# Performance work log

Hardware: AMD Instinct MI355X
Metric: run time of the kernel (lower is better)

Reference implementation:

```python
import jax, jax.numpy as jnp
import numpy as np

B, L, LH, D, H = 32, 512, 2048, 1024, 4
DK = D // H  # dot-attn head dim
NEG = -1e9


def _ln(x, g, b, eps=1e-5):
    m = x.mean(-1, keepdims=True)
    v = ((x - m) ** 2).mean(-1, keepdims=True)
    return (x - m) / jnp.sqrt(v + eps) * g + b


def setup_inputs() -> dict:
    key = jax.random.key(0)
    ks = jax.random.split(key, 16)
    s = 0.05
    inp = {
        "seq_emb": jax.random.normal(ks[0], (B, L, D), jnp.float32),
        "seq_mask": jnp.ones((B, L), jnp.float32),
        "his_seq_emb": jax.random.normal(ks[1], (B, LH, D), jnp.float32),
        "his_seq_mask": jnp.ones((B, LH), jnp.float32),
        # dot-product MHA (bias=True)
        "sa_wq": jax.random.normal(ks[2], (D, D), jnp.float32) * s,
        "sa_bq": jnp.zeros((D,), jnp.float32),
        "sa_wk": jax.random.normal(ks[3], (D, D), jnp.float32) * s,
        "sa_bk": jnp.zeros((D,), jnp.float32),
        "sa_wv": jax.random.normal(ks[4], (D, D), jnp.float32) * s,
        "sa_bv": jnp.zeros((D,), jnp.float32),
        "sa_wo": jax.random.normal(ks[5], (D, D), jnp.float32) * s,
        "sa_bo": jnp.zeros((D,), jnp.float32),
        # short LayerNorm
        "sn_g": jnp.ones((D,), jnp.float32),
        "sn_b": jnp.zeros((D,), jnp.float32),
        # additive MHA (h=1, bias=False)
        "aa_wq": jax.random.normal(ks[6], (D, D), jnp.float32) * s,
        "aa_wk": jax.random.normal(ks[7], (D, D), jnp.float32) * s,
        "aa_wv": jax.random.normal(ks[8], (D, D), jnp.float32) * s,
        "aa_wo": jax.random.normal(ks[9], (D, D), jnp.float32) * s,
        "aa_wa": jax.random.normal(ks[10], (D,), jnp.float32) * s,
        # long LayerNorm
        "ln_g": jnp.ones((D,), jnp.float32),
        "ln_b": jnp.zeros((D,), jnp.float32),
    }
    return inp


def reference(seq_emb, seq_mask, his_seq_emb, his_seq_mask,
              sa_wq, sa_bq, sa_wk, sa_bk, sa_wv, sa_bv, sa_wo, sa_bo,
              sn_g, sn_b, aa_wq, aa_wk, aa_wv, aa_wo, aa_wa, ln_g, ln_b):
    # ---- dot-product self attention over seq_emb (dropout = eval/no-op) ----
    def split_heads(x):  # (B,L,D) -> (B,H,L,DK)
        return x.reshape(B, -1, H, DK).transpose(0, 2, 1, 3)

    q = split_heads(seq_emb @ sa_wq + sa_bq)
    k = split_heads(seq_emb @ sa_wk + sa_bk)
    v = split_heads(seq_emb @ sa_wv + sa_bv)
    scores = jnp.einsum('bhqd,bhkd->bhqk', q, k) / jnp.sqrt(jnp.float32(DK))
    scores = jnp.where(seq_mask[:, None, None, :] == 0, NEG, scores)
    p_attn = jax.nn.softmax(scores, axis=-1)  # (B,H,L,L)
    ctx = jnp.einsum('bhqk,bhkd->bhqd', p_attn, v)
    ctx = ctx.transpose(0, 2, 1, 3).reshape(B, L, D)
    sa_out = ctx @ sa_wo + sa_bo

    poi_attn = _ln(sa_out, sn_g, sn_b) * seq_mask[:, :, None]
    poi_hidden = poi_attn.mean(axis=1, keepdims=True)  # (B,1,D)

    # ---- additive (Bahdanau) attention, h=1, Lq=1 ----
    aq = poi_hidden @ aa_wq        # (B,1,D)
    ak = his_seq_emb @ aa_wk       # (B,LH,D)
    av = his_seq_emb @ aa_wv       # (B,LH,D)
    feats = jnp.tanh(aq[:, :, None, :] + ak[:, None, :, :])  # (B,1,LH,D)
    a_scores = jnp.einsum('bqkd,d->bqk', feats, aa_wa)        # (B,1,LH)
    a_scores = jnp.where(his_seq_mask[:, None, :] == 0, NEG, a_scores)
    a_w = jax.nn.softmax(a_scores, axis=-1)
    a_ctx = jnp.einsum('bqk,bkd->bqd', a_w, av)               # (B,1,D)
    aa_out = a_ctx @ aa_wo

    his_poi_hidden = poi_hidden + _ln(aa_out, ln_g, ln_b)     # (B,1,D)

    attn_weight = p_attn[:, 0, :, :]                          # (B,L,L)
    seq_hidden = jnp.concatenate([poi_hidden, his_poi_hidden], axis=-1)[:, 0, :]  # (B,2D)
    return seq_hidden, attn_weight
```

## Files before the change

kernel.cpp:

```cpp
#include <hip/hip_runtime.h>

#define NEGV (-1000000000.0f)

typedef __attribute__((ext_vector_type(8))) short sh8;
typedef __attribute__((ext_vector_type(4))) short sh4;
typedef __attribute__((ext_vector_type(8))) __bf16 bf16x8;
typedef __attribute__((ext_vector_type(4))) float f32x4;

__device__ __forceinline__ float b2f(unsigned short u) {
  unsigned v = ((unsigned)u) << 16;
  return __builtin_bit_cast(float, v);
}
__device__ __forceinline__ unsigned short f2b(float f) {
  unsigned x = __builtin_bit_cast(unsigned, f);
  unsigned r = (x + 0x7fffu + ((x >> 16) & 1u)) >> 16;
  return (unsigned short)r;
}
__device__ __forceinline__ void g2l16(const void* g, void* l) {
  __builtin_amdgcn_global_load_lds((const __attribute__((address_space(1))) unsigned int*)g,
                                   (__attribute__((address_space(3))) unsigned int*)l, 16, 0, 0);
}
__device__ __forceinline__ f32x4 mfma16(bf16x8 a, bf16x8 b, f32x4 c) {
  return __builtin_amdgcn_mfma_f32_16x16x32_bf16(a, b, c, 0, 0, 0);
}
__device__ __forceinline__ float fast_tanh(float x) {
  x = fminf(fmaxf(x, -15.f), 15.f);
  float e = __expf(2.f * x);
  return (e - 1.f) / (e + 1.f);
}

__global__ void cvt_bf16(const float* __restrict__ src, unsigned short* __restrict__ dst, int n4) {
  int i = blockIdx.x * blockDim.x + threadIdx.x;
  int stride = gridDim.x * blockDim.x;
  for (; i < n4; i += stride) {
    float4 v = ((const float4*)src)[i];
    sh4 o;
    o[0] = (short)f2b(v.x); o[1] = (short)f2b(v.y);
    o[2] = (short)f2b(v.z); o[3] = (short)f2b(v.w);
    ((sh4*)dst)[i] = o;
  }
}

__global__ void tcvt(const float* __restrict__ src, unsigned short* __restrict__ dst) {
  __shared__ float tile[64][65];
  int bx = blockIdx.x, by = blockIdx.y;
  int tx = threadIdx.x & 63, ty = threadIdx.x >> 6;
#pragma unroll
  for (int i = 0; i < 16; ++i) {
    int r = i * 4 + ty;
    tile[r][tx] = src[(size_t)(by * 64 + r) * 1024 + bx * 64 + tx];
  }
  __syncthreads();
#pragma unroll
  for (int i = 0; i < 16; ++i) {
    int r = i * 4 + ty;
    dst[(size_t)(bx * 64 + r) * 1024 + by * 64 + tx] = f2b(tile[tx][r]);
  }
}

template<int EPI>
__global__ __launch_bounds__(512, 1)
void gemm256(const unsigned short* __restrict__ A, const unsigned short* __restrict__ Bt,
             int nbx,
             const float* __restrict__ b0, const float* __restrict__ b1,
             const float* __restrict__ b2,
             unsigned short* __restrict__ O0, unsigned short* __restrict__ O1,
             unsigned short* __restrict__ O2,
             const float* __restrict__ aq, const float* __restrict__ wa,
             float* __restrict__ sc)
{
  __shared__ char lds[131072];
  const int tid = threadIdx.x;
  const int w = tid >> 6, l = tid & 63;
  const int wm = w >> 2, wn = w & 3;
  const int lr = l & 15, g = l >> 4;
  const int swz = (lr >> 1) & 3;

  const int wg = blockIdx.x;
  const int cpx = gridDim.x >> 3;
  const int wgid = (wg & 7) * cpx + (wg >> 3);
  const int bx = wgid % nbx, by = wgid / nbx;
  const size_t m0 = (size_t)by * 256;
  const int n0 = bx * 256;

  f32x4 acc[8][4] = {};
  bf16x8 fa[2][8], fb[2][4];

  const int srow = tid >> 2;
  const int sk = (((tid & 3) ^ ((tid >> 3) & 3)) * 8);
  const unsigned short* gA = A + (m0 + srow) * 1024 + sk;
  const unsigned short* gB = Bt + ((size_t)n0 + srow) * 1024 + sk;
  char* const sbase = lds + w * 1024;

  const int aoff = (wm * 128 + lr) * 64 + ((g ^ swz) * 16);
  const int boff = 16384 + (wn * 64 + lr) * 64 + ((g ^ swz) * 16);

  auto stageAB = [&](int kt) {
    const unsigned short* a = gA + kt * 32;
    const unsigned short* b = gB + kt * 32;
    char* base = sbase + ((kt & 3) << 15);
    g2l16(a, base);
    g2l16(a + 128 * 1024, base + 8192);
    g2l16(b, base + 16384);
    g2l16(b + 128 * 1024, base + 24576);
  };

  stageAB(0); stageAB(1); stageAB(2);
  asm volatile("s_waitcnt vmcnt(4)" ::: "memory");
  __builtin_amdgcn_s_barrier();
  {
    const char* p0 = lds;
#pragma unroll
    for (int j = 0; j < 4; ++j) fb[0][j] = *(const bf16x8*)(p0 + boff + j * 1024);
#pragma unroll
    for (int i = 0; i < 8; ++i) fa[0][i] = *(const bf16x8*)(p0 + aoff + i * 1024);
  }
  __builtin_amdgcn_sched_barrier(0);

#define GITER(KTV, CUR, NXT)                                                   \
  {                                                                            \
    const int kt_ = (KTV);                                                     \
    if (kt_ < 29) stageAB(kt_ + 3);                                            \
    if (kt_ < 31) {                                                            \
      const char* pn_ = lds + (((kt_ + 1) & 3) << 15);                         \
      _Pragma("unroll")                                                        \
      for (int j = 0; j < 4; ++j)                                              \
        fb[NXT][j] = *(const bf16x8*)(pn_ + boff + j * 1024);                  \
      _Pragma("unroll")                                                        \
      for (int i = 0; i < 8; ++i)                                              \
        fa[NXT][i] = *(const bf16x8*)(pn_ + aoff + i * 1024);                  \
    }                                                                          \
    __builtin_amdgcn_sched_barrier(0);                                         \
    __builtin_amdgcn_s_setprio(1);                                             \
    _Pragma("unroll")                                                          \
    for (int i = 0; i < 8; ++i)                                                \
      _Pragma("unroll")                                                        \
      for (int j = 0; j < 4; ++j)                                              \
        acc[i][j] = mfma16(fa[CUR][i], fb[CUR][j], acc[i][j]);                 \
    __builtin_amdgcn_s_setprio(0);                                             \
    if (kt_ < 29) { asm volatile("s_waitcnt vmcnt(4)" ::: "memory"); }         \
    else if (kt_ == 29) { asm volatile("s_waitcnt vmcnt(0)" ::: "memory"); }   \
    if (kt_ < 31) __builtin_amdgcn_s_barrier();                                \
  }

#pragma unroll 1
  for (int kk = 0; kk < 28; kk += 2) {
    GITER(kk, 0, 1)
    GITER(kk + 1, 1, 0)
  }
  GITER(28, 0, 1)
  GITER(29, 1, 0)
  GITER(30, 0, 1)
  GITER(31, 1, 0)
#undef GITER

  if (EPI == 0) {
#pragma unroll
    for (int j = 0; j < 4; ++j) {
      int col = n0 + wn * 64 + j * 16 + lr;
      float bv = b0[col];
#pragma unroll
      for (int i = 0; i < 8; ++i) {
        size_t rowb = m0 + wm * 128 + i * 16 + g * 4;
#pragma unroll
        for (int r = 0; r < 4; ++r)
          O0[(rowb + r) * 1024 + col] = f2b(acc[i][j][r] + bv);
      }
    }
  } else if (EPI == 1) {
#pragma unroll
    for (int j = 0; j < 4; ++j) {
      int col3 = n0 + wn * 64 + j * 16 + lr;
      int part = col3 >> 10, c = col3 & 1023;
      float bv = (part == 0) ? b0[c] : (part == 1) ? b1[c] : b2[c];
      if (part < 2) {
        unsigned short* O = part == 0 ? O0 : O1;
#pragma unroll
        for (int i = 0; i < 8; ++i) {
          size_t rowb = m0 + wm * 128 + i * 16 + g * 4;
#pragma unroll
          for (int r = 0; r < 4; ++r)
            O[(rowb + r) * 1024 + c] = f2b(acc[i][j][r] + bv);
        }
      } else {
        int h = c >> 8, d = c & 255;
#pragma unroll
        for (int i = 0; i < 8; ++i) {
          size_t row = m0 + wm * 128 + i * 16 + g * 4;
          int bb = (int)(row >> 9), ll = (int)(row & 511);
          size_t base = ((size_t)(bb * 4 + h) * 256 + d) * 512 + ll;
#pragma unroll
          for (int r = 0; r < 4; ++r)
            O2[base + r] = f2b(acc[i][j][r] + bv);
        }
      }
    }
  } else {
    const int bb = (int)(m0 >> 11);
#pragma unroll
    for (int i = 0; i < 8; ++i) {
      float rp[4] = {0.f, 0.f, 0.f, 0.f};
#pragma unroll
      for (int j = 0; j < 4; ++j) {
        int col = n0 + wn * 64 + j * 16 + lr;
        float wav = wa[col];
        float aqv = aq[bb * 1024 + col];
#pragma unroll
        for (int r = 0; r < 4; ++r)
          rp[r] += wav * fast_tanh(acc[i][j][r] + aqv);
      }
#pragma unroll
      for (int off = 1; off < 16; off <<= 1)
#pragma unroll
        for (int r = 0; r < 4; ++r)
          rp[r] += __shfl_xor(rp[r], off, 64);
      if (lr == 0) {
        size_t rowb = m0 + wm * 128 + i * 16 + g * 4;
#pragma unroll
        for (int r = 0; r < 4; ++r)
          atomicAdd(&sc[rowb + r], rp[r]);
      }
    }
  }
}

__global__ __launch_bounds__(256, 4)
void attn_kernel(const unsigned short* __restrict__ q, const unsigned short* __restrict__ k,
                 const unsigned short* __restrict__ vT, const float* __restrict__ seq_mask,
                 unsigned short* __restrict__ ctx, float* __restrict__ attn_out)
{
  __shared__ char smem[34304];
  unsigned short* Qs = (unsigned short*)smem;
  unsigned short* Ps = (unsigned short*)smem;
  float* redm = (float*)(smem + 33280);
  float* reds = (float*)(smem + 33792);
  const int t = threadIdx.x, w = t >> 6, l = t & 63;
  const int lr = l & 15, g = l >> 4, lk8 = g * 8;
  const int wg = blockIdx.x;
  const int wgid = (wg & 7) * 256 + (wg >> 3);
  const int qt = wgid & 15, bh = wgid >> 4;
  const int h = bh & 3, b = bh >> 2;
  const int l0 = qt * 32;

  for (int idx = t; idx < 32 * 32; idx += 256) {
    int r = idx >> 5, ch = (idx & 31) * 8;
    *(sh8*)&Qs[r * 264 + ch] =
        *(const sh8*)&q[((size_t)(b * 512 + l0 + r)) * 1024 + h * 256 + ch];
  }
  __syncthreads();

  f32x4 accs[2][8] = {};
  const unsigned short* kbase = k + ((size_t)b * 512) * 1024 + h * 256;
#pragma unroll
  for (int ds = 0; ds < 8; ++ds) {
    int d0 = ds * 32;
    bf16x8 a0 = *(const bf16x8*)&Qs[lr * 264 + d0 + lk8];
    bf16x8 a1 = *(const bf16x8*)&Qs[(16 + lr) * 264 + d0 + lk8];
#pragma unroll
    for (int j = 0; j < 8; ++j) {
      int kj = w * 128 + j * 16 + lr;
      bf16x8 bb = *(const bf16x8*)&kbase[(size_t)kj * 1024 + d0 + lk8];
      accs[0][j] = mfma16(a0, bb, accs[0][j]);
      accs[1][j] = mfma16(a1, bb, accs[1][j]);
    }
  }

#pragma unroll
  for (int j = 0; j < 8; ++j) {
    int col = w * 128 + j * 16 + lr;
    float mv = seq_mask[b * 512 + col];
    bool msk = (mv == 0.f);
#pragma unroll
    for (int i = 0; i < 2; ++i)
#pragma unroll
      for (int r = 0; r < 4; ++r)
        accs[i][j][r] = msk ? NEGV : accs[i][j][r] * 0.0625f;
  }

  float mx[2][4], sm[2][4];
#pragma unroll
  for (int i = 0; i < 2; ++i)
#pragma unroll
    for (int r = 0; r < 4; ++r) {
      float m = accs[i][0][r];
#pragma unroll
      for (int j = 1; j < 8; ++j) m = fmaxf(m, accs[i][j][r]);
      mx[i][r] = m;
    }
#pragma unroll
  for (int off = 1; off < 16; off <<= 1)
#pragma unroll
    for (int i = 0; i < 2; ++i)
#pragma unroll
      for (int r = 0; r < 4; ++r)
        mx[i][r] = fmaxf(mx[i][r], __shfl_xor(mx[i][r], off, 64));
  if (lr == 0) {
#pragma unroll
    for (int i = 0; i < 2; ++i)
#pragma unroll
      for (int r = 0; r < 4; ++r)
        redm[w * 32 + i * 16 + g * 4 + r] = mx[i][r];
  }
  __syncthreads();
#pragma unroll
  for (int i = 0; i < 2; ++i)
#pragma unroll
    for (int r = 0; r < 4; ++r) {
      int row = i * 16 + g * 4 + r;
      mx[i][r] = fmaxf(fmaxf(redm[row], redm[32 + row]),
                       fmaxf(redm[64 + row], redm[96 + row]));
      sm[i][r] = 0.f;
    }

#pragma unroll
  for (int i = 0; i < 2; ++i)
#pragma unroll
    for (int j = 0; j < 8; ++j)
#pragma unroll
      for (int r = 0; r < 4; ++r) {
        float p = __expf(accs[i][j][r] - mx[i][r]);
        accs[i][j][r] = p;
        sm[i][r] += p;
      }
#pragma unroll
  for (int off = 1; off < 16; off <<= 1)
#pragma unroll
    for (int i = 0; i < 2; ++i)
#pragma unroll
      for (int r = 0; r < 4; ++r)
        sm[i][r] += __shfl_xor(sm[i][r], off, 64);
  if (lr == 0) {
#pragma unroll
    for (int i = 0; i < 2; ++i)
#pragma unroll
      for (int r = 0; r < 4; ++r)
        reds[w * 32 + i * 16 + g * 4 + r] = sm[i][r];
  }
  __syncthreads();
#pragma unroll
  for (int i = 0; i < 2; ++i)
#pragma unroll
    for (int r = 0; r < 4; ++r) {
      int row = i * 16 + g * 4 + r;
      float s = reds[row] + reds[32 + row] + reds[64 + row] + reds[96 + row];
      sm[i][r] = 1.f / s;
    }

#pragma unroll
  for (int i = 0; i < 2; ++i)
#pragma unroll
    for (int j = 0; j < 8; ++j) {
      int col = w * 128 + j * 16 + lr;
#pragma unroll
      for (int r = 0; r < 4; ++r) {
        int row = i * 16 + g * 4 + r;
        float pn = accs[i][j][r] * sm[i][r];
        Ps[row * 520 + col] = f2b(pn);
        if (h == 0)
          attn_out[((size_t)(b * 512 + l0 + row)) * 512 + col] = pn;
      }
    }
  __syncthreads();

  f32x4 acco[2][4] = {};
  const unsigned short* vbase = vT + ((size_t)(b * 4 + h)) * 256 * 512;
#pragma unroll
  for (int ks = 0; ks < 16; ++ks) {
    int kj0 = ks * 32;
    bf16x8 a0 = *(const bf16x8*)&Ps[lr * 520 + kj0 + lk8];
    bf16x8 a1 = *(const bf16x8*)&Ps[(16 + lr) * 520 + kj0 + lk8];
#pragma unroll
    for (int j = 0; j < 4; ++j) {
      int d = w * 64 + j * 16 + lr;
      bf16x8 bb = *(const bf16x8*)&vbase[(size_t)d * 512 + kj0 + lk8];
      acco[0][j] = mfma16(a0, bb, acco[0][j]);
      acco[1][j] = mfma16(a1, bb, acco[1][j]);
    }
  }
#pragma unroll
  for (int i = 0; i < 2; ++i)
#pragma unroll
    for (int j = 0; j < 4; ++j) {
      int col = w * 64 + j * 16 + lr;
#pragma unroll
      for (int r = 0; r < 4; ++r) {
        int row = i * 16 + g * 4 + r;
        ctx[((size_t)(b * 512 + l0 + row)) * 1024 + h * 256 + col] = f2b(acco[i][j][r]);
      }
    }
}

__global__ __launch_bounds__(256)
void ln_mean(const unsigned short* __restrict__ sa, const float* __restrict__ g,
             const float* __restrict__ bt, const float* __restrict__ mask,
             float* __restrict__ poi_sum)
{
  const int b = blockIdx.y, ch = blockIdx.x;
  const int t = threadIdx.x, w = t >> 6, l = t & 63;
  float gg[16], bb[16];
#pragma unroll
  for (int j = 0; j < 16; ++j) { gg[j] = g[l * 16 + j]; bb[j] = bt[l * 16 + j]; }
  float accv[16];
#pragma unroll
  for (int j = 0; j < 16; ++j) accv[j] = 0.f;
  for (int rr = 0; rr < 16; ++rr) {
    int row = ch * 64 + w * 16 + rr;
    const unsigned short* rp = sa + ((size_t)(b * 512 + row)) * 1024 + l * 16;
    float x[16];
    sh8 v0 = *(const sh8*)rp;
    sh8 v1 = *(const sh8*)(rp + 8);
#pragma unroll
    for (int j = 0; j < 8; ++j) {
      x[j] = b2f((unsigned short)v0[j]);
      x[8 + j] = b2f((unsigned short)v1[j]);
    }
    float s = 0.f, s2 = 0.f;
#pragma unroll
    for (int j = 0; j < 16; ++j) { s += x[j]; s2 += x[j] * x[j]; }
#pragma unroll
    for (int off = 1; off < 64; off <<= 1) {
      s += __shfl_xor(s, off, 64);
      s2 += __shfl_xor(s2, off, 64);
    }
    float mean = s * (1.f / 1024.f);
    float var = s2 * (1.f / 1024.f) - mean * mean;
    float rinv = rsqrtf(var + 1e-5f);
    float mk = mask[b * 512 + row];
#pragma unroll
    for (int j = 0; j < 16; ++j) accv[j] += ((x[j] - mean) * rinv * gg[j] + bb[j]) * mk;
  }
#pragma unroll
  for (int j = 0; j < 16; ++j) atomicAdd(&poi_sum[b * 1024 + l * 16 + j], accv[j]);
}

__global__ void finalize_poi(const float* __restrict__ ps, float* __restrict__ poi) {
  int i = blockIdx.x * 256 + threadIdx.x;
  if (i < 32 * 1024) poi[i] = ps[i] * (1.f / 512.f);
}

__global__ __launch_bounds__(256)
void gemv32(const float* __restrict__ in, const float* __restrict__ W, float* __restrict__ out)
{
  const int b = blockIdx.y;
  const int n = blockIdx.x * 256 + threadIdx.x;
  const float* ib = in + b * 1024;
  float acc = 0.f;
  for (int d = 0; d < 1024; d += 4) {
    acc += ib[d]     * W[(size_t)d * 1024 + n]
         + ib[d + 1] * W[(size_t)(d + 1) * 1024 + n]
         + ib[d + 2] * W[(size_t)(d + 2) * 1024 + n]
         + ib[d + 3] * W[(size_t)(d + 3) * 1024 + n];
  }
  out[b * 1024 + n] = acc;
}

__global__ __launch_bounds__(256)
void softmax_his(float* __restrict__ sc, const float* __restrict__ mask)
{
  __shared__ float red[4];
  const int b = blockIdx.x, t = threadIdx.x, w = t >> 6, l = t & 63;
  float v[8];
  float mx = -3.0e38f;
#pragma unroll
  for (int i = 0; i < 8; ++i) {
    int kk = t + i * 256;
    float s = (mask[b * 2048 + kk] == 0.f) ? NEGV : sc[b * 2048 + kk];
    v[i] = s;
    mx = fmaxf(mx, s);
  }
#pragma unroll
  for (int off = 1; off < 64; off <<= 1) mx = fmaxf(mx, __shfl_xor(mx, off, 64));
  if (l == 0) red[w] = mx;
  __syncthreads();
  mx = fmaxf(fmaxf(red[0], red[1]), fmaxf(red[2], red[3]));
  float sum = 0.f;
#pragma unroll
  for (int i = 0; i < 8; ++i) { v[i] = __expf(v[i] - mx); sum += v[i]; }
#pragma unroll
  for (int off = 1; off < 64; off <<= 1) sum += __shfl_xor(sum, off, 64);
  __syncthreads();
  if (l == 0) red[w] = sum;
  __syncthreads();
  sum = red[0] + red[1] + red[2] + red[3];
  float inv = 1.f / sum;
#pragma unroll
  for (int i = 0; i < 8; ++i) sc[b * 2048 + t + i * 256] = v[i] * inv;
}

__global__ __launch_bounds__(256)
void hw_kernel(const float* __restrict__ aw, const unsigned short* __restrict__ his,
               float* __restrict__ hw)
{
  const int b = blockIdx.y, kc = blockIdx.x, t = threadIdx.x;
  const int cb = t * 4;
  float a0 = 0.f, a1 = 0.f, a2 = 0.f, a3 = 0.f;
  for (int kk = 0; kk < 256; ++kk) {
    int k = kc * 256 + kk;
    float wg = aw[b * 2048 + k];
    sh4 vv = *(const sh4*)&his[((size_t)(b * 2048 + k)) * 1024 + cb];
    a0 += wg * b2f((unsigned short)vv[0]);
    a1 += wg * b2f((unsigned short)vv[1]);
    a2 += wg * b2f((unsigned short)vv[2]);
    a3 += wg * b2f((unsigned short)vv[3]);
  }
  atomicAdd(&hw[b * 1024 + cb + 0], a0);
  atomicAdd(&hw[b * 1024 + cb + 1], a1);
  atomicAdd(&hw[b * 1024 + cb + 2], a2);
  atomicAdd(&hw[b * 1024 + cb + 3], a3);
}

__global__ __launch_bounds__(256)
void final_kernel(const float* __restrict__ aa_out, const float* __restrict__ g,
                  const float* __restrict__ bt, const float* __restrict__ poi,
                  float* __restrict__ out)
{
  __shared__ float r1[4], r2[4];
  const int b = blockIdx.x, t = threadIdx.x, w = t >> 6, l = t & 63;
  float x[4];
#pragma unroll
  for (int j = 0; j < 4; ++j) x[j] = aa_out[b * 1024 + t * 4 + j];
  float s = 0.f, s2 = 0.f;
#pragma unroll
  for (int j = 0; j < 4; ++j) { s += x[j]; s2 += x[j] * x[j]; }
#pragma unroll
  for (int off = 1; off < 64; off <<= 1) {
    s += __shfl_xor(s, off, 64);
    s2 += __shfl_xor(s2, off, 64);
  }
  if (l == 0) { r1[w] = s; r2[w] = s2; }
  __syncthreads();
  s = r1[0] + r1[1] + r1[2] + r1[3];
  s2 = r2[0] + r2[1] + r2[2] + r2[3];
  float mean = s * (1.f / 1024.f);
  float var = s2 * (1.f / 1024.f) - mean * mean;
  float rinv = rsqrtf(var + 1e-5f);
#pragma unroll
  for (int j = 0; j < 4; ++j) {
    int c = t * 4 + j;
    float lnv = (x[j] - mean) * rinv * g[c] + bt[c];
    float pv = poi[b * 1024 + c];
    out[b * 2048 + c] = pv;
    out[b * 2048 + 1024 + c] = pv + lnv;
  }
}

extern "C" void kernel_launch(void* const* d_in, const int* in_sizes, int n_in,
                              void* d_out, int out_size, void* d_ws, size_t ws_size,
                              hipStream_t stream)
{
  const float* seq_emb  = (const float*)d_in[0];
  const float* seq_mask = (const float*)d_in[1];
  const float* his_emb  = (const float*)d_in[2];
  const float* his_mask = (const float*)d_in[3];
  const float* sa_wq = (const float*)d_in[4];
  const float* sa_bq = (const float*)d_in[5];
  const float* sa_wk = (const float*)d_in[6];
  const float* sa_bk = (const float*)d_in[7];
  const float* sa_wv = (const float*)d_in[8];
  const float* sa_bv = (const float*)d_in[9];
  const float* sa_wo = (const float*)d_in[10];
  const float* sa_bo = (const float*)d_in[11];
  const float* sn_g  = (const float*)d_in[12];
  const float* sn_b  = (const float*)d_in[13];
  const float* aa_wq = (const float*)d_in[14];
  const float* aa_wk = (const float*)d_in[15];
  const float* aa_wv = (const float*)d_in[16];
  const float* aa_wo = (const float*)d_in[17];
  const float* aa_wa = (const float*)d_in[18];
  const float* ln_g  = (const float*)d_in[19];
  const float* ln_b  = (const float*)d_in[20];
  float* out = (float*)d_out;

  char* p = (char*)d_ws;
  size_t off = 0;
  auto alloc = [&](size_t bytes) -> void* {
    void* r = p + off;
    off += (bytes + 255) & ~(size_t)255;
    return r;
  };
  unsigned short* seqb = (unsigned short*)alloc((size_t)16384 * 1024 * 2);
  unsigned short* hisb = (unsigned short*)alloc((size_t)65536 * 1024 * 2);
  unsigned short* wcat = (unsigned short*)alloc((size_t)3072 * 1024 * 2);
  unsigned short* woT  = (unsigned short*)alloc((size_t)1024 * 1024 * 2);
  unsigned short* awkT = (unsigned short*)alloc((size_t)1024 * 1024 * 2);
  unsigned short* qb   = (unsigned short*)alloc((size_t)16384 * 1024 * 2);
  unsigned short* kb   = (unsigned short*)alloc((size_t)16384 * 1024 * 2);
  unsigned short* vTb  = (unsigned short*)alloc((size_t)16384 * 1024 * 2);
  unsigned short* ctxb = (unsigned short*)alloc((size_t)16384 * 1024 * 2);
  unsigned short* saob = (unsigned short*)alloc((size_t)16384 * 1024 * 2);
  float* poi_sum = (float*)alloc((size_t)32 * 1024 * 4);
  float* poi     = (float*)alloc((size_t)32 * 1024 * 4);
  float* aqb     = (float*)alloc((size_t)32 * 1024 * 4);
  float* ascore  = (float*)alloc((size_t)32 * 2048 * 4);
  float* hwb     = (float*)alloc((size_t)32 * 1024 * 4);
  float* actx    = (float*)alloc((size_t)32 * 1024 * 4);
  float* aaout   = (float*)alloc((size_t)32 * 1024 * 4);
  if (off > ws_size) return;

  hipMemsetAsync(poi_sum, 0, (size_t)32 * 1024 * 4, stream);
  hipMemsetAsync(ascore, 0, (size_t)32 * 2048 * 4, stream);
  hipMemsetAsync(hwb, 0, (size_t)32 * 1024 * 4, stream);

  cvt_bf16<<<2048, 256, 0, stream>>>(seq_emb, seqb, 16384 * 1024 / 4);
  cvt_bf16<<<2048, 256, 0, stream>>>(his_emb, hisb, 65536 * 1024 / 4);
  dim3 tg(16, 16);
  tcvt<<<tg, 256, 0, stream>>>(sa_wq, wcat);
  tcvt<<<tg, 256, 0, stream>>>(sa_wk, wcat + (size_t)1024 * 1024);
  tcvt<<<tg, 256, 0, stream>>>(sa_wv, wcat + (size_t)2048 * 1024);
  tcvt<<<tg, 256, 0, stream>>>(sa_wo, woT);
  tcvt<<<tg, 256, 0, stream>>>(aa_wk, awkT);

  gemm256<1><<<768, 512, 0, stream>>>(seqb, wcat, 12, sa_bq, sa_bk, sa_bv,
                                      qb, kb, vTb, nullptr, nullptr, nullptr);

  attn_kernel<<<2048, 256, 0, stream>>>(qb, kb, vTb, seq_mask, ctxb, out + 65536);

  gemm256<0><<<256, 512, 0, stream>>>(ctxb, woT, 4, sa_bo, nullptr, nullptr,
                                      saob, nullptr, nullptr, nullptr, nullptr, nullptr);
  ln_mean<<<dim3(8, 32), 256, 0, stream>>>(saob, sn_g, sn_b, seq_mask, poi_sum);
  finalize_poi<<<128, 256, 0, stream>>>(poi_sum, poi);
  gemv32<<<dim3(4, 32), 256, 0, stream>>>(poi, aa_wq, aqb);

  gemm256<2><<<1024, 512, 0, stream>>>(hisb, awkT, 4, nullptr, nullptr, nullptr,
                                       nullptr, nullptr, nullptr, aqb, aa_wa, ascore);
  softmax_his<<<32, 256, 0, stream>>>(ascore, his_mask);
  hw_kernel<<<dim3(8, 32), 256, 0, stream>>>(ascore, hisb, hwb);
  gemv32<<<dim3(4, 32), 256, 0, stream>>>(hwb, aa_wv, actx);
  gemv32<<<dim3(4, 32), 256, 0, stream>>>(actx, aa_wo, aaout);
  final_kernel<<<32, 256, 0, stream>>>(aaout, ln_g, ln_b, poi, out);
}
```

Measured before the change: 802.6 us.

## Restructure GEMM mainloop into 8-phase double-buffered K=64 pipeline with interleaved staging

Replaces the 4-stage K=32 pipeline with a two-buffer K=64 tile scheme. Each buffer is split into eight phases, and each phase loads half the A fragments plus B fragments, issues a slice of the next tile's global-to-LDS copies, then runs 16 MFMAs between barriers. The LDS layout changes to 128-byte rows with an 8-way XOR swizzle. The aim is to spread global loads evenly across the compute and cut fragment register pressure. In exchange it adds more barriers per K tile and tighter manual wait-count bookkeeping.

```diff
diff --git a/kernel.cpp b/kernel.cpp
--- a/kernel.cpp
+++ b/kernel.cpp
@@ -74,7 +74,6 @@
   const int w = tid >> 6, l = tid & 63;
   const int wm = w >> 2, wn = w & 3;
   const int lr = l & 15, g = l >> 4;
-  const int swz = (lr >> 1) & 3;
 
   const int wg = blockIdx.x;
   const int cpx = gridDim.x >> 3;
@@ -84,75 +83,75 @@
   const int n0 = bx * 256;
 
   f32x4 acc[8][4] = {};
-  bf16x8 fa[2][8], fb[2][4];
-
-  const int srow = tid >> 2;
-  const int sk = (((tid & 3) ^ ((tid >> 3) & 3)) * 8);
-  const unsigned short* gA = A + (m0 + srow) * 1024 + sk;
-  const unsigned short* gB = Bt + ((size_t)n0 + srow) * 1024 + sk;
-  char* const sbase = lds + w * 1024;
-
-  const int aoff = (wm * 128 + lr) * 64 + ((g ^ swz) * 16);
-  const int boff = 16384 + (wn * 64 + lr) * 64 + ((g ^ swz) * 16);
-
-  auto stageAB = [&](int kt) {
-    const unsigned short* a = gA + kt * 32;
-    const unsigned short* b = gB + kt * 32;
-    char* base = sbase + ((kt & 3) << 15);
-    g2l16(a, base);
-    g2l16(a + 128 * 1024, base + 8192);
-    g2l16(b, base + 16384);
-    g2l16(b + 128 * 1024, base + 24576);
-  };
-
-  stageAB(0); stageAB(1); stageAB(2);
-  asm volatile("s_waitcnt vmcnt(4)" ::: "memory");
-  __builtin_amdgcn_s_barrier();
-  {
-    const char* p0 = lds;
-#pragma unroll
-    for (int j = 0; j < 4; ++j) fb[0][j] = *(const bf16x8*)(p0 + boff + j * 1024);
-#pragma unroll
-    for (int i = 0; i < 8; ++i) fa[0][i] = *(const bf16x8*)(p0 + aoff + i * 1024);
-  }
-  __builtin_amdgcn_sched_barrier(0);
-
-#define GITER(KTV, CUR, NXT)                                                   \
-  {                                                                            \
-    const int kt_ = (KTV);                                                     \
-    if (kt_ < 29) stageAB(kt_ + 3);                                            \
-    if (kt_ < 31) {                                                            \
-      const char* pn_ = lds + (((kt_ + 1) & 3) << 15);                         \
-      _Pragma("unroll")                                                        \
-      for (int j = 0; j < 4; ++j)                                              \
-        fb[NXT][j] = *(const bf16x8*)(pn_ + boff + j * 1024);                  \
-      _Pragma("unroll")                                                        \
-      for (int i = 0; i < 8; ++i)                                              \
-        fa[NXT][i] = *(const bf16x8*)(pn_ + aoff + i * 1024);                  \
-    }                                                                          \
-    __builtin_amdgcn_sched_barrier(0);                                         \
-    __builtin_amdgcn_s_setprio(1);                                             \
-    _Pragma("unroll")                                                          \
-    for (int i = 0; i < 8; ++i)                                                \
-      _Pragma("unroll")                                                        \
-      for (int j = 0; j < 4; ++j)                                              \
-        acc[i][j] = mfma16(fa[CUR][i], fb[CUR][j], acc[i][j]);                 \
-    __builtin_amdgcn_s_setprio(0);                                             \
-    if (kt_ < 29) { asm volatile("s_waitcnt vmcnt(4)" ::: "memory"); }         \
-    else if (kt_ == 29) { asm volatile("s_waitcnt vmcnt(0)" ::: "memory"); }   \
-    if (kt_ < 31) __builtin_amdgcn_s_barrier();                                \
-  }
+  bf16x8 fa[4], fb[4];
+
+  const int srow = w * 8 + (l >> 3);
+  const int schunk = ((l & 7) ^ ((l >> 3) & 7)) * 8;
+  const unsigned short* gA = A + (m0 + srow) * 1024 + schunk;
+  const unsigned short* gB = Bt + ((size_t)n0 + srow) * 1024 + schunk;
+  const int ldst = w * 1024;
+
+  const int chs = lr & 7;
+  const int aRd0 = wm * 16384 + lr * 128;
+  const int bRd0 = 32768 + (wn >> 1) * 16384 + (wn & 1) * 8192 + lr * 128;
+  const int ck0 = ((0 * 4 + g) ^ chs) * 16;
+  const int ck1 = ((1 * 4 + g) ^ chs) * 16;
+
+#define STG_A(BUF, AH, RH, KK) \
+  g2l16(gA + ((AH) * 128 + (RH) * 64) * 1024 + (KK), \
+        lds + (BUF) * 65536 + (AH) * 16384 + (RH) * 8192 + ldst)
+#define STG_B(BUF, BH, RH, KK) \
+  g2l16(gB + ((BH) * 128 + (RH) * 64) * 1024 + (KK), \
+        lds + (BUF) * 65536 + 32768 + (BH) * 16384 + (RH) * 8192 + ldst)
+
+#define PH(BUFOFF, CK, IH, STAGES, TAIL)                                      \
+  {                                                                           \
+    const char* pb_ = lds + (BUFOFF);                                         \
+    if ((IH) == 0) {                                                          \
+      _Pragma("unroll") for (int j = 0; j < 4; ++j)                           \
+        fb[j] = *(const bf16x8*)(pb_ + bRd0 + j * 2048 + (CK));               \
+    }                                                                         \
+    _Pragma("unroll") for (int i = 0; i < 4; ++i)                             \
+      fa[i] = *(const bf16x8*)(pb_ + aRd0 + (IH) * 8192 + i * 2048 + (CK));   \
+    STAGES;                                                                   \
+    __builtin_amdgcn_sched_barrier(0);                                        \
+    asm volatile("s_barrier" ::: "memory");                                   \
+    asm volatile("s_waitcnt lgkmcnt(0)" ::: "memory");                        \
+    __builtin_amdgcn_sched_barrier(0);                                        \
+    __builtin_amdgcn_s_setprio(1);                                            \
+    _Pragma("unroll") for (int i = 0; i < 4; ++i)                             \
+      _Pragma("unroll") for (int j = 0; j < 4; ++j)                           \
+        acc[(IH) * 4 + i][j] = mfma16(fa[i], fb[j], acc[(IH) * 4 + i][j]);    \
+    __builtin_amdgcn_s_setprio(0);                                            \
+    TAIL;                                                                     \
+    asm volatile("s_barrier" ::: "memory");                                   \
+  }
+
+  STG_A(0, 0, 0, 0); STG_A(0, 0, 1, 0); STG_A(0, 1, 0, 0); STG_A(0, 1, 1, 0);
+  STG_B(0, 0, 0, 0); STG_B(0, 0, 1, 0); STG_B(0, 1, 0, 0); STG_B(0, 1, 1, 0);
+  STG_A(1, 0, 0, 64); STG_A(1, 1, 0, 64);
+  asm volatile("s_waitcnt vmcnt(0)" ::: "memory");
+  asm volatile("s_barrier" ::: "memory");
 
 #pragma unroll 1
-  for (int kk = 0; kk < 28; kk += 2) {
-    GITER(kk, 0, 1)
-    GITER(kk + 1, 1, 0)
-  }
-  GITER(28, 0, 1)
-  GITER(29, 1, 0)
-  GITER(30, 0, 1)
-  GITER(31, 1, 0)
-#undef GITER
+  for (int t = 0; t < 8; ++t) {
+    const int k1 = (2 * t + 1) * 64, k2 = (2 * t + 2) * 64, k3 = (2 * t + 3) * 64;
+    const bool st = (t < 7);
+    PH(0,     ck0, 0, { STG_A(1, 0, 1, k1); STG_A(1, 1, 1, k1); }, {})
+    PH(0,     ck0, 1, { STG_B(1, 0, 0, k1); STG_B(1, 0, 1, k1); }, {})
+    PH(0,     ck1, 0, { STG_B(1, 1, 0, k1); STG_B(1, 1, 1, k1); }, {})
+    PH(0,     ck1, 1, { if (st) { STG_A(0, 0, 0, k2); STG_A(0, 1, 0, k2); } },
+       { if (st) { asm volatile("s_waitcnt vmcnt(2)" ::: "memory"); }
+         else    { asm volatile("s_waitcnt vmcnt(0)" ::: "memory"); } })
+    PH(65536, ck0, 0, { if (st) { STG_A(0, 0, 1, k2); STG_A(0, 1, 1, k2); } }, {})
+    PH(65536, ck0, 1, { if (st) { STG_B(0, 0, 0, k2); STG_B(0, 0, 1, k2); } }, {})
+    PH(65536, ck1, 0, { if (st) { STG_B(0, 1, 0, k2); STG_B(0, 1, 1, k2); } }, {})
+    PH(65536, ck1, 1, { if (st) { STG_A(1, 0, 0, k3); STG_A(1, 1, 0, k3); } },
+       { if (st) { asm volatile("s_waitcnt vmcnt(2)" ::: "memory"); } })
+  }
+#undef PH
+#undef STG_A
+#undef STG_B
 
   if (EPI == 0) {
 #pragma unroll
```

Measured after the change: 784.3 us. 2.3% less time.
